# Performance work log

Hardware: AMD Instinct MI355X
Metric: run time of the kernel (lower is better)

Reference implementation:

```python
import jax, jax.numpy as jnp
import numpy as np
from jax import lax

N = 50000      # nodes
E = 1600000    # edges
F = 128        # input features
G = 32         # gnn_hidden_dim
H = 50         # lstm hidden_dim
SEQ = 10       # sequence_length


def setup_inputs() -> dict:
    key = jax.random.key(0)
    ks = jax.random.split(key, 12)
    s = 0.05
    return {
        "x": jax.random.normal(ks[0], (N, F), jnp.float32),
        "W_gcn": jax.random.normal(ks[1], (F, G), jnp.float32) * s,
        "b_gcn": jnp.zeros((G,), jnp.float32),
        "w_ih0": jax.random.normal(ks[2], (4 * H, G), jnp.float32) * s,
        "w_hh0": jax.random.normal(ks[3], (4 * H, H), jnp.float32) * s,
        "b_ih0": jnp.zeros((4 * H,), jnp.float32),
        "b_hh0": jnp.zeros((4 * H,), jnp.float32),
        "w_ih1": jax.random.normal(ks[4], (4 * H, H), jnp.float32) * s,
        "w_hh1": jax.random.normal(ks[5], (4 * H, H), jnp.float32) * s,
        "b_ih1": jnp.zeros((4 * H,), jnp.float32),
        "b_hh1": jnp.zeros((4 * H,), jnp.float32),
        "fc_w": jax.random.normal(ks[6], (1, H), jnp.float32) * s,
        "fc_b": jnp.zeros((1,), jnp.float32),
        "edge_index": jax.random.randint(ks[7], (2, E), 0, N, dtype=jnp.int64),
        "seq_len": SEQ,
    }


def gcn_conv(x, edge_index, W, b):
    # PyG GCNConv: add self-loops, symmetric deg^{-1/2} normalization,
    # linear transform, gather-scale-scatter aggregation at target nodes.
    n = x.shape[0]
    loop = jnp.arange(n, dtype=edge_index.dtype)
    src = jnp.concatenate([edge_index[0], loop])  # message sources j
    dst = jnp.concatenate([edge_index[1], loop])  # aggregation targets i
    deg = jax.ops.segment_sum(jnp.ones_like(dst, dtype=x.dtype), dst,
                              num_segments=n)
    dinv = jnp.where(deg > 0, lax.rsqrt(jnp.maximum(deg, 1.0)), 0.0)
    norm = dinv[src] * dinv[dst]                       # [E+N]
    h = x @ W                                          # [N, G]
    msg = h[src] * norm[:, None]                       # gather + scale
    out = jax.ops.segment_sum(msg, dst, num_segments=n)
    return out + b


def lstm_layer(x_proj, w_hh, b_hh):
    # x_proj: [T, B, 4H] precomputed input projections (i,f,g,o gate order).
    T, B, H4 = x_proj.shape
    Hd = H4 // 4
    h0 = jnp.zeros((B, Hd), x_proj.dtype)
    c0 = jnp.zeros((B, Hd), x_proj.dtype)

    def step(carry, xp):
        h, c = carry
        gates = xp + h @ w_hh.T + b_hh
        i, f, g, o = jnp.split(gates, 4, axis=-1)
        i, f, o = jax.nn.sigmoid(i), jax.nn.sigmoid(f), jax.nn.sigmoid(o)
        g = jnp.tanh(g)
        c = f * c + i * g
        h = o * jnp.tanh(c)
        return (h, c), h

    (h, c), ys = lax.scan(step, (h0, c0), x_proj)
    return ys, h


def reference(x, W_gcn, b_gcn, w_ih0, w_hh0, b_ih0, b_hh0,
              w_ih1, w_hh1, b_ih1, b_hh1, fc_w, fc_b,
              edge_index, seq_len):
    gnn_out = gcn_conv(x, edge_index, W_gcn, b_gcn)        # [N, G]
    # lstm_in = gnn_out repeated seq_len times -> input projection is
    # identical per step; compute once and broadcast (same math).
    p0 = gnn_out @ w_ih0.T + b_ih0                         # [N, 4H]
    x_proj0 = jnp.broadcast_to(p0, (seq_len,) + p0.shape)  # [T, N, 4H]
    ys0, _ = lstm_layer(x_proj0, w_hh0, b_hh0)             # [T, N, H]
    x_proj1 = ys0 @ w_ih1.T + b_ih1                        # [T, N, 4H]
    _, hn1 = lstm_layer(x_proj1, w_hh1, b_hh1)             # [N, H]
    return hn1 @ fc_w.T + fc_b                             # [N, 1]
```

## Files before the change

### kernel.cpp

```cpp
#include <hip/hip_runtime.h>
#include <hip/hip_bf16.h>

typedef __attribute__((ext_vector_type(8))) short short8;
typedef __attribute__((ext_vector_type(4))) float f32x4;

#define L2E 1.442695041f
#define SCAN_B 256

__device__ __forceinline__ short f2bf(float f) {
  union { __hip_bfloat16 b; short s; } u;
  u.b = __float2bfloat16(f);
  return u.s;
}
__device__ __forceinline__ float b2f(short s) {
  unsigned u = ((unsigned)(unsigned short)s) << 16;
  return __uint_as_float(u);
}

__device__ __forceinline__ float ldh(const float* p, size_t i) { return p[i]; }
__device__ __forceinline__ float ldh(const __hip_bfloat16* p, size_t i) {
  return __bfloat162float(p[i]);
}
__device__ __forceinline__ void sth(float* p, size_t i, float v) { p[i] = v; }
__device__ __forceinline__ void sth(__hip_bfloat16* p, size_t i, float v) {
  p[i] = __float2bfloat16(v);
}

__device__ __forceinline__ short8 load_gfrag(const float* g, size_t base) {
  const float4* gp = (const float4*)(g + base);
  float4 a = gp[0], b = gp[1];
  short8 t;
  t[0]=f2bf(a.x); t[1]=f2bf(a.y); t[2]=f2bf(a.z); t[3]=f2bf(a.w);
  t[4]=f2bf(b.x); t[5]=f2bf(b.y); t[6]=f2bf(b.z); t[7]=f2bf(b.w);
  return t;
}
__device__ __forceinline__ short8 load_gfrag(const __hip_bfloat16* g, size_t base) {
  return *(const short8*)(g + base);
}

#define OFF_WIH0 0
#define OFF_WHH0 13312
#define OFF_WIH1 39936
#define OFF_WHH1 66560
#define OFF_B0   93184
#define OFF_B1   94016
#define OFF_FCW  94848
#define IMG_BYTES 95104

__global__ void k_detect(const int* __restrict__ ei, int E, int* __restrict__ flag) {
  if (threadIdx.x == 0 && blockIdx.x == 0) {
    int odd_nz = 0, even_nz = 0;
    int m = min(128, E);
    for (int i = 0; i < m; ++i) {
      odd_nz |= (ei[2 * i + 1] != 0);
      even_nz |= (ei[2 * i] != 0);
    }
    *flag = (even_nz && !odd_nz) ? 1 : 0;
  }
}


__global__ void k_count(const int* __restrict__ ei, int E,
                        const int* __restrict__ flag, int* __restrict__ cnt) {
  int e = blockIdx.x * blockDim.x + threadIdx.x;
  if (e < E) {
    int d = (*flag) ? ei[2 * (E + e)] : ei[E + e];
    atomicAdd(&cnt[d], 1);
  }
}

__global__ void k_convert(const int* __restrict__ ei, int E,
                          unsigned int* __restrict__ ed, int* __restrict__ cnt) {
  __shared__ int sflag;
  if (threadIdx.x == 0) {
    int odd_nz = 0, even_nz = 0;
    int m = min(128, E);
    for (int i = 0; i < m; ++i) {
      odd_nz |= (ei[2 * i + 1] != 0);
      even_nz |= (ei[2 * i] != 0);
    }
    sflag = (even_nz && !odd_nz) ? 1 : 0;
  }
  __syncthreads();
  int is64 = sflag;
  int e = blockIdx.x * blockDim.x + threadIdx.x;
  if (e < E) {
    int s = is64 ? ei[2 * e] : ei[e];
    int d = is64 ? ei[2 * (E + e)] : ei[E + e];
    ed[e] = (unsigned int)s | ((unsigned int)d << 16);
    atomicAdd(&cnt[d], 1);
  }
}

__global__ void k_dinv(const int* __restrict__ cnt, float* __restrict__ dinv, int N) {
  int i = blockIdx.x * blockDim.x + threadIdx.x;
  if (i < N) dinv[i] = rsqrtf((float)cnt[i] + 1.0f);
}

__global__ __launch_bounds__(256) void k_scanA(const int* __restrict__ cnt,
                                               float* __restrict__ dinv,
                                               int* __restrict__ bsum, int N) {
  __shared__ int red[256];
  int b = blockIdx.x, t = threadIdx.x;
  int chunk = (N + SCAN_B - 1) / SCAN_B;
  int lo = b * chunk, hi = min(lo + chunk, N);
  int s = 0;
  for (int i = lo + t; i < hi; i += 256) {
    int c = cnt[i];
    dinv[i] = rsqrtf((float)c + 1.0f);
    s += c;
  }
  red[t] = s;
  __syncthreads();
  for (int o = 128; o > 0; o >>= 1) {
    if (t < o) red[t] += red[t + o];
    __syncthreads();
  }
  if (t == 0) bsum[b] = red[0];
}

__global__ __launch_bounds__(256) void k_scanB(int* __restrict__ a,
                                               const int* __restrict__ bsum,
                                               int N) {
  __shared__ int sh[256];
  int b = blockIdx.x, t = threadIdx.x;
  int chunk = (N + SCAN_B - 1) / SCAN_B;
  int lo = b * chunk, hi = min(lo + chunk, N);
  sh[t] = bsum[t];
  __syncthreads();
  for (int o = 1; o < 256; o <<= 1) {
    int u = (t >= o) ? sh[t - o] : 0;
    __syncthreads();
    sh[t] += u;
    __syncthreads();
  }
  int carry = (b == 0) ? 0 : sh[b - 1];
  __syncthreads();
  for (int i0 = lo; i0 < hi; i0 += 256) {
    int i = i0 + t;
    int c = (i < hi) ? a[i] : 0;
    sh[t] = c;
    __syncthreads();
    for (int o = 1; o < 256; o <<= 1) {
      int u = (t >= o) ? sh[t - o] : 0;
      __syncthreads();
      sh[t] += u;
      __syncthreads();
    }
    if (i < hi) a[i] = carry + sh[t] - c;
    carry += sh[255];
    __syncthreads();
  }
}

__global__ void k_fill_p(const unsigned int* __restrict__ ed, int E,
                         int* __restrict__ rowst,
                         unsigned short* __restrict__ csr, int lo, int hi) {
  int e = blockIdx.x * blockDim.x + threadIdx.x;
  if (e < E) {
    unsigned int v = ed[e];
    int d = (int)(v >> 16);
    if (d >= lo && d < hi) {
      int p = atomicAdd(&rowst[d], 1);
      csr[p] = (unsigned short)(v & 0xFFFFu);
    }
  }
}

template <typename CT>
__global__ void k_fill(const int* __restrict__ ei, int E,
                       const int* __restrict__ flag,
                       int* __restrict__ rowst, CT* __restrict__ csr,
                       int lo, int hi) {
  int e = blockIdx.x * blockDim.x + threadIdx.x;
  if (e < E) {
    int is64 = *flag;
    int d = is64 ? ei[2 * (E + e)] : ei[E + e];
    if (d >= lo && d < hi) {
      int s = is64 ? ei[2 * e] : ei[e];
      int p = atomicAdd(&rowst[d], 1);
      csr[p] = (CT)s;
    }
  }
}

template <typename HT>
__global__ __launch_bounds__(256) void k_hs(const float* __restrict__ x,
                                            const float* __restrict__ Wg,
                                            const float* __restrict__ dinv,
                                            HT* __restrict__ hs, int N) {
  __shared__ __align__(16) float xt[64][132];
  __shared__ __align__(16) float Wl[128][32];
  int tid = threadIdx.x;
  int nb = blockIdx.x * 64;
  for (int i = tid; i < 4096; i += 256) Wl[i >> 5][i & 31] = Wg[i];
  const float4* xv = (const float4*)x;
  for (int i = tid; i < 2048; i += 256) {
    int r = i >> 5, c = i & 31;
    float4 v = make_float4(0.f, 0.f, 0.f, 0.f);
    if (nb + r < N) v = xv[(size_t)(nb + r) * 32 + c];
    *(float4*)&xt[r][c * 4] = v;
  }
  __syncthreads();
  int nl = tid >> 2, gq = (tid & 3) * 8;
  float a[8];
#pragma unroll
  for (int j = 0; j < 8; ++j) a[j] = 0.f;
  for (int k = 0; k < 128; ++k) {
    float xk = xt[nl][k];
#pragma unroll
    for (int j = 0; j < 8; ++j) a[j] += xk * Wl[k][gq + j];
  }
  int n = nb + nl;
  if (n < N) {
    float d = dinv[n];
#pragma unroll
    for (int j = 0; j < 8; ++j) sth(hs, (size_t)n * 32 + gq + j, a[j] * d);
  }
}

template <typename HT, typename GT, typename CT>
__global__ void k_gather(const CT* __restrict__ csr, const int* __restrict__ rowst,
                         const HT* __restrict__ hs, const float* __restrict__ dinv,
                         const float* __restrict__ bg, GT* __restrict__ gout,
                         int N) {
  int w = (blockIdx.x * blockDim.x + threadIdx.x) >> 6;
  if (w >= N) return;
  int l = threadIdx.x & 63;
  int g = l & 31, j = l >> 5;
  int end = rowst[w];
  int start = (w == 0) ? 0 : rowst[w - 1];
  int deg = end - start;
  int dmax = min(deg, 64);
  int idx = (l < deg) ? (int)csr[start + l] : 0;
  float acc = 0.0f;
#pragma unroll 1
  for (int base = 0; base < 64; base += 16) {
    if (base >= dmax) break;
#pragma unroll
    for (int i = 0; i < 8; ++i) {
      int e = base + 2 * i + j;
      int src = __shfl(idx, e);
      float v = ldh(hs, (size_t)src * 32 + g);
      acc += (e < dmax) ? v : 0.0f;
    }
  }
  for (int k = start + 64 + j; k < end; k += 2)
    acc += ldh(hs, (size_t)csr[k] * 32 + g);
  acc += __shfl_xor(acc, 32);
  if (j == 0) {
    float v = (acc + ldh(hs, (size_t)w * 32 + g)) * dinv[w] + bg[g];
    sth(gout, (size_t)w * 32 + g, v);
  }
}

template <typename HT>
__global__ void k_scatter(const int* __restrict__ ei, int E,
                          const int* __restrict__ flag,
                          const HT* __restrict__ hs, float* __restrict__ gout) {
  long long gid = (long long)blockIdx.x * blockDim.x + threadIdx.x;
  int e = (int)(gid >> 3), part = (int)(gid & 7);
  if (e >= E) return;
  int is64 = *flag;
  int s = is64 ? ei[2 * e] : ei[e];
  int d = is64 ? ei[2 * (E + e)] : ei[E + e];
  int b = part * 4;
  float* gp = gout + (size_t)d * 32 + b;
  size_t hp = (size_t)s * 32 + b;
  atomicAdd(gp + 0, ldh(hs, hp + 0));
  atomicAdd(gp + 1, ldh(hs, hp + 1));
  atomicAdd(gp + 2, ldh(hs, hp + 2));
  atomicAdd(gp + 3, ldh(hs, hp + 3));
}
template <typename HT>
__global__ void k_finish(const HT* __restrict__ hs, const float* __restrict__ dinv,
                         const float* __restrict__ bg, float* __restrict__ gout,
                         int N) {
  int gid = blockIdx.x * blockDim.x + threadIdx.x;
  if (gid < N * 32) {
    int n = gid >> 5, g = gid & 31;
    gout[gid] = (gout[gid] + ldh(hs, (size_t)gid)) * dinv[n] + bg[g];
  }
}

__global__ void k_prep(const float* __restrict__ wih0, const float* __restrict__ whh0,
                       const float* __restrict__ wih1, const float* __restrict__ whh1,
                       const float* __restrict__ bih0, const float* __restrict__ bhh0,
                       const float* __restrict__ bih1, const float* __restrict__ bhh1,
                       const float* __restrict__ fcw, unsigned char* __restrict__ img,
                       int* __restrict__ rowst, int N) {
  int gid = blockIdx.x * blockDim.x + threadIdx.x;
  int nthr = gridDim.x * blockDim.x;
  for (int i = gid; i < N; i += nthr) rowst[i] = 0;
  {
    short* W = (short*)(img + OFF_WIH0);
    for (int i = gid; i < 208 * 32; i += nthr) {
      int row = i >> 5, k = i & 31, u = row >> 2, q = row & 3;
      float sc = (q == 2) ? 2.0f * L2E : -L2E;
      float v = (u < 50) ? wih0[(q * 50 + u) * 32 + k] * sc : 0.0f;
      W[row * 32 + (k ^ ((row & 3) << 3))] = f2bf(v);
    }
  }
  {
    short* W = (short*)(img + OFF_WHH0);
    for (int i = gid; i < 208 * 64; i += nthr) {
      int row = i >> 6, k = i & 63, u = row >> 2, q = row & 3;
      float sc = (q == 2) ? 2.0f * L2E : -L2E;
      float v = (u < 50 && k < 50) ? whh0[(q * 50 + u) * 50 + k] * sc : 0.0f;
      W[row * 64 + (k ^ ((row & 7) << 3))] = f2bf(v);
    }
  }
  {
    short* W = (short*)(img + OFF_WIH1);
    for (int i = gid; i < 208 * 64; i += nthr) {
      int row = i >> 6, k = i & 63, u = row >> 2, q = row & 3;
      float sc = (q == 2) ? 2.0f * L2E : -L2E;
      float v = (u < 50 && k < 50) ? wih1[(q * 50 + u) * 50 + k] * sc : 0.0f;
      W[row * 64 + (k ^ ((row & 7) << 3))] = f2bf(v);
    }
  }
  {
    short* W = (short*)(img + OFF_WHH1);
    for (int i = gid; i < 208 * 64; i += nthr) {
      int row = i >> 6, k = i & 63, u = row >> 2, q = row & 3;
      float sc = (q == 2) ? 2.0f * L2E : -L2E;
      float v = (u < 50 && k < 50) ? whh1[(q * 50 + u) * 50 + k] * sc : 0.0f;
      W[row * 64 + (k ^ ((row & 7) << 3))] = f2bf(v);
    }
  }
  {
    float* B = (float*)(img + OFF_B0);
    for (int i = gid; i < 208; i += nthr) {
      int u = i >> 2, q = i & 3;
      float sc = (q == 2) ? 2.0f * L2E : -L2E;
      B[i] = (u < 50) ? (bih0[q * 50 + u] + bhh0[q * 50 + u]) * sc : 0.0f;
    }
  }
  {
    float* B = (float*)(img + OFF_B1);
    for (int i = gid; i < 208; i += nthr) {
      int u = i >> 2, q = i & 3;
      float sc = (q == 2) ? 2.0f * L2E : -L2E;
      B[i] = (u < 50) ? (bih1[q * 50 + u] + bhh1[q * 50 + u]) * sc : 0.0f;
    }
  }
  {
    float* F = (float*)(img + OFF_FCW);
    for (int i = gid; i < 64; i += nthr) F[i] = (i < 50) ? fcw[i] : 0.0f;
  }
}

__device__ __forceinline__ float gate_update(const f32x4& acc, float& cp) {
  float ei = __builtin_amdgcn_exp2f(acc[0]);
  float ef = __builtin_amdgcn_exp2f(acc[1]);
  float eo = __builtin_amdgcn_exp2f(acc[3]);
  float eg = __builtin_amdgcn_exp2f(fminf(acc[2], 80.0f));
  float a = 1.0f + ei, b = 1.0f + ef;
  float rif = __builtin_amdgcn_rcpf(a * b);
  float iv = rif * b, fv = rif * a;
  float o1 = 1.0f + eo, g1 = eg + 1.0f;
  float rog = __builtin_amdgcn_rcpf(o1 * g1);
  float ov = rog * g1;
  float gv = (eg - 1.0f) * (rog * o1);
  float c = fv * cp + iv * gv;
  cp = c;
  float Ec = __builtin_amdgcn_exp2f(c * (2.0f * L2E));
  float th = (Ec - 1.0f) * __builtin_amdgcn_rcpf(Ec + 1.0f);
  return ov * th;
}

template <typename GT>
__global__ __launch_bounds__(512, 2) void k_lstm(const GT* __restrict__ gout,
    const unsigned char* __restrict__ img, const float* __restrict__ fcb_p,
    float* __restrict__ out, int N) {
  __shared__ __align__(16) unsigned char smem[160640];
  const int tid = threadIdx.x;
  {
    const uint4* s = (const uint4*)img;
    uint4* d = (uint4*)smem;
    for (int i = tid; i < IMG_BYTES / 16; i += 512) d[i] = s[i];
  }
  __syncthreads();
  const int lane = tid & 63, wid = tid >> 6;
  const int l15 = lane & 15, l4 = lane >> 4;
  const int swz7 = (l15 & 7) << 3, swz3 = (l15 & 3) << 3;
  const int node0 = blockIdx.x * 256 + wid * 32;

  const short* WIH0 = (const short*)(smem + OFF_WIH0);
  const short* WHH0 = (const short*)(smem + OFF_WHH0);
  const short* WIH1 = (const short*)(smem + OFF_WIH1);
  const short* WHH1 = (const short*)(smem + OFF_WHH1);
  const float* B0   = (const float*)(smem + OFF_B0);
  const float* B1   = (const float*)(smem + OFF_B1);
  const float* FCW  = (const float*)(smem + OFF_FCW);
  short* h0st = (short*)(smem + IMG_BYTES + wid * 8192);
  short* h1st = h0st + 2048;

  {
    uint4 z; z.x = z.y = z.z = z.w = 0u;
    uint4* p = (uint4*)h0st;
    for (int i = lane; i < 512; i += 64) p[i] = z;
  }

  f32x4 p0r[13][2];
  {
    short8 gfrag[2];
#pragma unroll
    for (int v = 0; v < 2; ++v) {
      int node = node0 + v * 16 + l15;
      short8 t = {0, 0, 0, 0, 0, 0, 0, 0};
      if (node < N) t = load_gfrag(gout, (size_t)node * 32 + l4 * 8);
      gfrag[v] = t;
    }
#pragma unroll
    for (int t = 0; t < 13; ++t) {
      short8 w = *(const short8*)(WIH0 + (16 * t + l15) * 32 + ((l4 * 8) ^ swz3));
      f32x4 bv = *(const f32x4*)(B0 + t * 16 + l4 * 4);
#pragma unroll
      for (int v = 0; v < 2; ++v)
        p0r[t][v] = __builtin_amdgcn_mfma_f32_16x16x32_bf16(w, gfrag[v], bv, 0, 0, 0);
    }
  }

  float c0[13][2], c1[13][2];
#pragma unroll
  for (int t = 0; t < 13; ++t) { c0[t][0]=0.f; c0[t][1]=0.f; c1[t][0]=0.f; c1[t][1]=0.f; }

#pragma unroll 1
  for (int s = 0; s < 10; ++s) {
    short8 h0f[2][2], h1f[2][2];
#pragma unroll
    for (int c = 0; c < 2; ++c)
#pragma unroll
      for (int v = 0; v < 2; ++v) {
        int nl = v * 16 + l15;
        h0f[c][v] = *(const short8*)(h0st + nl * 64 + ((c * 32 + l4 * 8) ^ swz7));
        h1f[c][v] = *(const short8*)(h1st + nl * 64 + ((c * 32 + l4 * 8) ^ swz7));
      }
#pragma unroll
    for (int t = 0; t < 13; ++t) {
      int arow = (16 * t + l15);
      short8 ah0 = *(const short8*)(WHH0 + arow * 64 + ((l4 * 8) ^ swz7));
      short8 ah1 = *(const short8*)(WHH0 + arow * 64 + ((32 + l4 * 8) ^ swz7));
#pragma unroll
      for (int v = 0; v < 2; ++v) {
        f32x4 acc = p0r[t][v];
        acc = __builtin_amdgcn_mfma_f32_16x16x32_bf16(ah0, h0f[0][v], acc, 0, 0, 0);
        acc = __builtin_amdgcn_mfma_f32_16x16x32_bf16(ah1, h0f[1][v], acc, 0, 0, 0);
        float h = gate_update(acc, c0[t][v]);
        h0st[(v * 16 + l15) * 64 + ((4 * t + l4) ^ swz7)] = f2bf(h);
      }
    }
    short8 h0nf[2][2];
#pragma unroll
    for (int c = 0; c < 2; ++c)
#pragma unroll
      for (int v = 0; v < 2; ++v) {
        int nl = v * 16 + l15;
        h0nf[c][v] = *(const short8*)(h0st + nl * 64 + ((c * 32 + l4 * 8) ^ swz7));
      }
#pragma unroll
    for (int t = 0; t < 13; ++t) {
      f32x4 bv = *(const f32x4*)(B1 + t * 16 + l4 * 4);
      int arow = (16 * t + l15);
      short8 ai0 = *(const short8*)(WIH1 + arow * 64 + ((l4 * 8) ^ swz7));
      short8 ai1 = *(const short8*)(WIH1 + arow * 64 + ((32 + l4 * 8) ^ swz7));
      short8 ah0 = *(const short8*)(WHH1 + arow * 64 + ((l4 * 8) ^ swz7));
      short8 ah1 = *(const short8*)(WHH1 + arow * 64 + ((32 + l4 * 8) ^ swz7));
#pragma unroll
      for (int v = 0; v < 2; ++v) {
        f32x4 acc = bv;
        acc = __builtin_amdgcn_mfma_f32_16x16x32_bf16(ai0, h0nf[0][v], acc, 0, 0, 0);
        acc = __builtin_amdgcn_mfma_f32_16x16x32_bf16(ai1, h0nf[1][v], acc, 0, 0, 0);
        acc = __builtin_amdgcn_mfma_f32_16x16x32_bf16(ah0, h1f[0][v], acc, 0, 0, 0);
        acc = __builtin_amdgcn_mfma_f32_16x16x32_bf16(ah1, h1f[1][v], acc, 0, 0, 0);
        float h = gate_update(acc, c1[t][v]);
        h1st[(v * 16 + l15) * 64 + ((4 * t + l4) ^ swz7)] = f2bf(h);
      }
    }
  }
  float fcb = fcb_p[0];
#pragma unroll
  for (int v = 0; v < 2; ++v) {
    int nl = v * 16 + l15;
    float facc = 0.f;
#pragma unroll
    for (int c = 0; c < 2; ++c) {
      short8 f = *(const short8*)(h1st + nl * 64 + ((c * 32 + l4 * 8) ^ swz7));
#pragma unroll
      for (int j = 0; j < 8; ++j)
        facc += b2f(f[j]) * FCW[c * 32 + l4 * 8 + j];
    }
    facc += __shfl_xor(facc, 16);
    facc += __shfl_xor(facc, 32);
    int node = node0 + v * 16 + l15;
    if (l4 == 0 && node < N) out[node] = facc + fcb;
  }
}

extern "C" void kernel_launch(void* const* d_in, const int* in_sizes, int n_in,
                              void* d_out, int out_size, void* d_ws, size_t ws_size,
                              hipStream_t stream) {
  const float* x    = (const float*)d_in[0];
  const float* Wg   = (const float*)d_in[1];
  const float* bg   = (const float*)d_in[2];
  const float* wih0 = (const float*)d_in[3];
  const float* whh0 = (const float*)d_in[4];
  const float* bih0 = (const float*)d_in[5];
  const float* bhh0 = (const float*)d_in[6];
  const float* wih1 = (const float*)d_in[7];
  const float* whh1 = (const float*)d_in[8];
  const float* bih1 = (const float*)d_in[9];
  const float* bhh1 = (const float*)d_in[10];
  const float* fcw  = (const float*)d_in[11];
  const float* fcb  = (const float*)d_in[12];
  const int*   edge = (const int*)d_in[13];
  int N = in_sizes[0] / 128;
  int E = in_sizes[13] / 2;

  char* ws = (char*)d_ws;
  size_t off = 0;
  auto take = [&](size_t b) {
    size_t o = off;
    off = (off + b + 255) & ~(size_t)255;
    return o;
  };
  int*   rowst = (int*)(ws + take((size_t)N * 4));
  float* dinv  = (float*)(ws + take((size_t)N * 4));
  int*   flag  = (int*)(ws + take(256));
  unsigned char* wimg = (unsigned char*)(ws + take(IMG_BYTES));
  size_t base = off;

  const int NP = 2;
  int span = (N + NP - 1) / NP;
  bool canU16 = (N <= 65535) && (E <= 100000000);

  size_t csr_b  = ((size_t)E * 2 + 255) & ~(size_t)255;
  size_t hsb    = ((size_t)N * 64 + 255) & ~(size_t)255;
  size_t reg2_b = (size_t)E * 4 > 2 * hsb ? (size_t)E * 4 : 2 * hsb;
  size_t needP  = base + csr_b + reg2_b;
  size_t needA = base + (((size_t)N * 128 + 255) & ~(size_t)255)
               + (((size_t)E * 4 + 255) & ~(size_t)255)
               + ((size_t)N * 128);

  k_prep<<<52, 256, 0, stream>>>(wih0, whh0, wih1, whh1, bih0, bhh0, bih1, bhh1,
                                 fcw, wimg, rowst, N);

  if (ws_size >= needA) {
    float* gout = (float*)(ws + take((size_t)N * 128));
    int*   csr  = (int*)(ws + take((size_t)E * 4));
    float* hs   = (float*)(ws + take((size_t)N * 128));
    int*   bsum = (int*)csr;
    k_detect<<<1, 1, 0, stream>>>(edge, E, flag);
    k_count<<<(E + 255) / 256, 256, 0, stream>>>(edge, E, flag, rowst);
    k_scanA<<<SCAN_B, 256, 0, stream>>>(rowst, dinv, bsum, N);
    k_scanB<<<SCAN_B, 256, 0, stream>>>(rowst, bsum, N);
    k_hs<float><<<(N + 63) / 64, 256, 0, stream>>>(x, Wg, dinv, hs, N);
    for (int p = 0; p < NP; ++p) {
      int lo = p * span, hi = min(lo + span, N);
      if (lo >= hi) break;
      k_fill<int><<<(E + 255) / 256, 256, 0, stream>>>(edge, E, flag, rowst,
                                                       csr, lo, hi);
    }
    k_gather<float, float, int><<<(N + 3) / 4, 256, 0, stream>>>(
        csr, rowst, hs, dinv, bg, gout, N);
    k_lstm<float><<<(N + 255) / 256, 512, 0, stream>>>(gout, wimg, fcb,
                                                       (float*)d_out, N);
  } else if (canU16 && ws_size >= needP) {
    unsigned short* csr = (unsigned short*)(ws + take(csr_b));
    char* reg2 = ws + take(reg2_b);
    unsigned int*   ed   = (unsigned int*)reg2;
    __hip_bfloat16* hs   = (__hip_bfloat16*)reg2;
    __hip_bfloat16* gout = (__hip_bfloat16*)(reg2 + hsb);
    int* bsum = (int*)csr;

    k_convert<<<(E + 255) / 256, 256, 0, stream>>>(edge, E, ed, rowst);
    k_scanA<<<SCAN_B, 256, 0, stream>>>(rowst, dinv, bsum, N);
    k_scanB<<<SCAN_B, 256, 0, stream>>>(rowst, bsum, N);
    for (int p = 0; p < NP; ++p) {
      int lo = p * span, hi = min(lo + span, N);
      if (lo >= hi) break;
      k_fill_p<<<(E + 255) / 256, 256, 0, stream>>>(ed, E, rowst, csr, lo, hi);
    }
    k_hs<__hip_bfloat16><<<(N + 63) / 64, 256, 0, stream>>>(x, Wg, dinv, hs, N);
    k_gather<__hip_bfloat16, __hip_bfloat16, unsigned short>
        <<<(N + 3) / 4, 256, 0, stream>>>(csr, rowst, hs, dinv, bg, gout, N);
    k_lstm<__hip_bfloat16><<<(N + 255) / 256, 512, 0, stream>>>(gout, wimg, fcb,
                                                                (float*)d_out, N);
  } else {
    float* gout = (float*)(ws + take((size_t)N * 128));
    __hip_bfloat16* hs = (__hip_bfloat16*)(ws + take((size_t)N * 64));
    hipMemsetAsync(gout, 0, (size_t)N * 128, stream);
    k_detect<<<1, 1, 0, stream>>>(edge, E, flag);
    k_count<<<(E + 255) / 256, 256, 0, stream>>>(edge, E, flag, rowst);
    k_dinv<<<(N + 255) / 256, 256, 0, stream>>>(rowst, dinv, N);
    k_hs<__hip_bfloat16><<<(N + 63) / 64, 256, 0, stream>>>(x, Wg, dinv, hs, N);
    int sc_blocks = (int)(((long long)E * 8 + 255) / 256);
    k_scatter<__hip_bfloat16><<<sc_blocks, 256, 0, stream>>>(edge, E, flag, hs, gout);
    k_finish<__hip_bfloat16><<<(N * 32 + 255) / 256, 256, 0, stream>>>(
        hs, dinv, bg, gout, N);
    k_lstm<float><<<(N + 255) / 256, 512, 0, stream>>>(gout, wimg, fcb,
                                                       (float*)d_out, N);
  }
}
```

Measured before the change: 349.9 us.

## Fuse CSR build into cooperative kernel, process four nodes per gather wave

Replaces the convert, two scan kernels and the partitioned fill launches with a single cooperative kernel that uses grid-wide syncs between the count, degree/dinv, prefix-scan and fill phases. This removes several launches and the gaps between them. The gather kernel now handles four destination nodes per wave, sharing one rowst load and shuffling the row bounds. The fill partition count rises from 2 to 4, and the compact u16/bf16 path is now preferred over the fp32 path whenever N fits. Risks include grid.sync cost on 512 blocks, a serial prefix over bsum in every block, and lower bf16 precision on the chosen path.

```diff
diff --git a/kernel.cpp b/kernel.cpp
--- a/kernel.cpp
+++ b/kernel.cpp
@@ -1,5 +1,8 @@
 #include <hip/hip_runtime.h>
 #include <hip/hip_bf16.h>
+#include <hip/hip_cooperative_groups.h>
+
+namespace cg = cooperative_groups;
 
 typedef __attribute__((ext_vector_type(8))) short short8;
 typedef __attribute__((ext_vector_type(4))) float f32x4;
@@ -56,6 +59,105 @@
       even_nz |= (ei[2 * i] != 0);
     }
     *flag = (even_nz && !odd_nz) ? 1 : 0;
+  }
+}
+
+__global__ __launch_bounds__(256) void k_edges(const int* __restrict__ ei,
+    int E, int N, int* __restrict__ rowst, float* __restrict__ dinv,
+    int* __restrict__ bsum, unsigned int* __restrict__ ed,
+    unsigned short* __restrict__ csr, int NP) {
+  cg::grid_group grid = cg::this_grid();
+  const int tid = threadIdx.x, b = blockIdx.x, GB = gridDim.x;
+  const int T = GB * 256;
+  const int gid = b * 256 + tid;
+  __shared__ int sh[256];
+  __shared__ int sflag;
+
+  for (int i = gid; i < N; i += T) rowst[i] = 0;
+  if (tid == 0) {
+    int odd_nz = 0, even_nz = 0;
+    int m = min(128, E);
+    for (int i = 0; i < m; ++i) {
+      odd_nz |= (ei[2 * i + 1] != 0);
+      even_nz |= (ei[2 * i] != 0);
+    }
+    sflag = (even_nz && !odd_nz) ? 1 : 0;
+  }
+  __syncthreads();
+  int is64 = sflag;
+  grid.sync();
+
+  for (int e = gid; e < E; e += T) {
+    int s = is64 ? ei[2 * e] : ei[e];
+    int d = is64 ? ei[2 * (E + e)] : ei[E + e];
+    ed[e] = (unsigned int)s | ((unsigned int)d << 16);
+    atomicAdd(&rowst[d], 1);
+  }
+  grid.sync();
+
+  const int chunk = (N + GB - 1) / GB;
+  const int lo = b * chunk, hi = min(lo + chunk, N);
+  {
+    int s = 0;
+    for (int i = lo + tid; i < hi; i += 256) {
+      int c = rowst[i];
+      dinv[i] = rsqrtf((float)c + 1.0f);
+      s += c;
+    }
+    sh[tid] = s;
+    __syncthreads();
+    for (int o = 128; o > 0; o >>= 1) {
+      if (tid < o) sh[tid] += sh[tid + o];
+      __syncthreads();
+    }
+    if (tid == 0) bsum[b] = sh[0];
+    __syncthreads();
+  }
+  grid.sync();
+
+  {
+    int part = 0;
+    for (int i = tid; i < b; i += 256) part += bsum[i];
+    sh[tid] = part;
+    __syncthreads();
+    for (int o = 128; o > 0; o >>= 1) {
+      if (tid < o) sh[tid] += sh[tid + o];
+      __syncthreads();
+    }
+    int carry = sh[0];
+    __syncthreads();
+    for (int i0 = lo; i0 < hi; i0 += 256) {
+      int i = i0 + tid;
+      int c = (i < hi) ? rowst[i] : 0;
+      sh[tid] = c;
+      __syncthreads();
+      for (int o = 1; o < 256; o <<= 1) {
+        int u = (tid >= o) ? sh[tid - o] : 0;
+        __syncthreads();
+        sh[tid] += u;
+        __syncthreads();
+      }
+      if (i < hi) rowst[i] = carry + sh[tid] - c;
+      carry += sh[255];
+      __syncthreads();
+    }
+  }
+  grid.sync();
+
+  const int span = (N + NP - 1) / NP;
+  for (int p = 0; p < NP; ++p) {
+    int wlo = p * span, whi = min(wlo + span, N);
+    if (wlo < whi) {
+      for (int e = gid; e < E; e += T) {
+        unsigned int v = ed[e];
+        int d = (int)(v >> 16);
+        if (d >= wlo && d < whi) {
+          int pos = atomicAdd(&rowst[d], 1);
+          csr[pos] = (unsigned short)(v & 0xFFFFu);
+        }
+      }
+    }
+    if (p + 1 < NP) grid.sync();
   }
 }
 
@@ -220,37 +322,54 @@
 }
 
 template <typename HT, typename GT, typename CT>
-__global__ void k_gather(const CT* __restrict__ csr, const int* __restrict__ rowst,
-                         const HT* __restrict__ hs, const float* __restrict__ dinv,
-                         const float* __restrict__ bg, GT* __restrict__ gout,
-                         int N) {
-  int w = (blockIdx.x * blockDim.x + threadIdx.x) >> 6;
-  if (w >= N) return;
+__global__ void k_gather4(const CT* __restrict__ csr, const int* __restrict__ rowst,
+                          const HT* __restrict__ hs, const float* __restrict__ dinv,
+                          const float* __restrict__ bg, GT* __restrict__ gout,
+                          int N) {
+  long long gtid = (long long)blockIdx.x * blockDim.x + threadIdx.x;
+  int wave = (int)(gtid >> 6);
+  int n0 = wave * 4;
+  if (n0 >= N) return;
   int l = threadIdx.x & 63;
-  int g = l & 31, j = l >> 5;
-  int end = rowst[w];
-  int start = (w == 0) ? 0 : rowst[w - 1];
-  int deg = end - start;
-  int dmax = min(deg, 64);
-  int idx = (l < deg) ? (int)csr[start + l] : 0;
-  float acc = 0.0f;
+  int gf = l & 31, j = l >> 5;
+  int rr = 0;
+  int ri = n0 - 1 + l;
+  if (l <= 4 && ri >= 0 && ri < N) rr = rowst[ri];
+  int st[4], en[4], idx[4], deg[4];
+#pragma unroll
+  for (int q = 0; q < 4; ++q) {
+    st[q] = __shfl(rr, q);
+    en[q] = __shfl(rr, q + 1);
+    deg[q] = en[q] - st[q];
+  }
+#pragma unroll
+  for (int q = 0; q < 4; ++q)
+    idx[q] = (n0 + q < N && l < deg[q]) ? (int)csr[st[q] + l] : 0;
+  float bgv = bg[gf];
+#pragma unroll
+  for (int q = 0; q < 4; ++q) {
+    int w = n0 + q;
+    if (w >= N) break;
+    float acc = 0.f;
+    int dm = min(deg[q], 64);
 #pragma unroll 1
-  for (int base = 0; base < 64; base += 16) {
-    if (base >= dmax) break;
-#pragma unroll
-    for (int i = 0; i < 8; ++i) {
-      int e = base + 2 * i + j;
-      int src = __shfl(idx, e);
-      float v = ldh(hs, (size_t)src * 32 + g);
-      acc += (e < dmax) ? v : 0.0f;
-    }
-  }
-  for (int k = start + 64 + j; k < end; k += 2)
-    acc += ldh(hs, (size_t)csr[k] * 32 + g);
-  acc += __shfl_xor(acc, 32);
-  if (j == 0) {
-    float v = (acc + ldh(hs, (size_t)w * 32 + g)) * dinv[w] + bg[g];
-    sth(gout, (size_t)w * 32 + g, v);
+    for (int base = 0; base < 64; base += 16) {
+      if (base >= dm) break;
+#pragma unroll
+      for (int i = 0; i < 8; ++i) {
+        int e = base + 2 * i + j;
+        int src = __shfl(idx[q], e);
+        float v = ldh(hs, (size_t)src * 32 + gf);
+        acc += (e < dm) ? v : 0.f;
+      }
+    }
+    for (int k2 = st[q] + 64 + j; k2 < en[q]; k2 += 2)
+      acc += ldh(hs, (size_t)csr[k2] * 32 + gf);
+    acc += __shfl_xor(acc, 32);
+    if (j == 0) {
+      float v = (acc + ldh(hs, (size_t)w * 32 + gf)) * dinv[w] + bgv;
+      sth(gout, (size_t)w * 32 + gf, v);
+    }
   }
 }
 
@@ -531,7 +650,7 @@
   unsigned char* wimg = (unsigned char*)(ws + take(IMG_BYTES));
   size_t base = off;
 
-  const int NP = 2;
+  const int NP = 4;
   int span = (N + NP - 1) / NP;
   bool canU16 = (N <= 65535) && (E <= 100000000);
 
@@ -543,10 +662,19 @@
                + (((size_t)E * 4 + 255) & ~(size_t)255)
                + ((size_t)N * 128);
 
+  int coop = 0;
+  {
+    int dev = 0;
+    hipDeviceProp_t prop;
+    if (hipGetDevice(&dev) == hipSuccess &&
+        hipGetDeviceProperties(&prop, dev) == hipSuccess)
+      coop = prop.cooperativeLaunch;
+  }
+
   k_prep<<<52, 256, 0, stream>>>(wih0, whh0, wih1, whh1, bih0, bhh0, bih1, bhh1,
                                  fcw, wimg, rowst, N);
 
-  if (ws_size >= needA) {
+  if (ws_size >= needA && !canU16) {
     float* gout = (float*)(ws + take((size_t)N * 128));
     int*   csr  = (int*)(ws + take((size_t)E * 4));
     float* hs   = (float*)(ws + take((size_t)N * 128));
@@ -562,7 +690,8 @@
       k_fill<int><<<(E + 255) / 256, 256, 0, stream>>>(edge, E, flag, rowst,
                                                        csr, lo, hi);
     }
-    k_gather<float, float, int><<<(N + 3) / 4, 256, 0, stream>>>(
+    int gwaves = (N + 3) / 4;
+    k_gather4<float, float, int><<<(gwaves * 64 + 255) / 256, 256, 0, stream>>>(
         csr, rowst, hs, dinv, bg, gout, N);
     k_lstm<float><<<(N + 255) / 256, 512, 0, stream>>>(gout, wimg, fcb,
                                                        (float*)d_out, N);
@@ -574,19 +703,51 @@
     __hip_bfloat16* gout = (__hip_bfloat16*)(reg2 + hsb);
     int* bsum = (int*)csr;
 
-    k_convert<<<(E + 255) / 256, 256, 0, stream>>>(edge, E, ed, rowst);
+    if (coop) {
+      int NPc = NP;
+      void* kargs[] = { (void*)&edge, (void*)&E, (void*)&N, (void*)&rowst,
+                        (void*)&dinv, (void*)&bsum, (void*)&ed, (void*)&csr,
+                        (void*)&NPc };
+      hipLaunchCooperativeKernel((void*)k_edges, dim3(512), dim3(256), kargs,
+                                 0, stream);
+    } else {
+      k_convert<<<(E + 255) / 256, 256, 0, stream>>>(edge, E, ed, rowst);
+      k_scanA<<<SCAN_B, 256, 0, stream>>>(rowst, dinv, bsum, N);
+      k_scanB<<<SCAN_B, 256, 0, stream>>>(rowst, bsum, N);
+      for (int p = 0; p < NP; ++p) {
+        int lo = p * span, hi = min(lo + span, N);
+        if (lo >= hi) break;
+        k_fill_p<<<(E + 255) / 256, 256, 0, stream>>>(ed, E, rowst, csr, lo, hi);
+      }
+    }
+    k_hs<__hip_bfloat16><<<(N + 63) / 64, 256, 0, stream>>>(x, Wg, dinv, hs, N);
+    int gwaves = (N + 3) / 4;
+    k_gather4<__hip_bfloat16, __hip_bfloat16, unsigned short>
+        <<<(gwaves * 64 + 255) / 256, 256, 0, stream>>>(csr, rowst, hs, dinv,
+                                                        bg, gout, N);
+    k_lstm<__hip_bfloat16><<<(N + 255) / 256, 512, 0, stream>>>(gout, wimg, fcb,
+                                                                (float*)d_out, N);
+  } else if (ws_size >= needA) {
+    float* gout = (float*)(ws + take((size_t)N * 128));
+    int*   csr  = (int*)(ws + take((size_t)E * 4));
+    float* hs   = (float*)(ws + take((size_t)N * 128));
+    int*   bsum = (int*)csr;
+    k_detect<<<1, 1, 0, stream>>>(edge, E, flag);
+    k_count<<<(E + 255) / 256, 256, 0, stream>>>(edge, E, flag, rowst);
     k_scanA<<<SCAN_B, 256, 0, stream>>>(rowst, dinv, bsum, N);
     k_scanB<<<SCAN_B, 256, 0, stream>>>(rowst, bsum, N);
+    k_hs<float><<<(N + 63) / 64, 256, 0, stream>>>(x, Wg, dinv, hs, N);
     for (int p = 0; p < NP; ++p) {
       int lo = p * span, hi = min(lo + span, N);
       if (lo >= hi) break;
-      k_fill_p<<<(E + 255) / 256, 256, 0, stream>>>(ed, E, rowst, csr, lo, hi);
-    }
-    k_hs<__hip_bfloat16><<<(N + 63) / 64, 256, 0, stream>>>(x, Wg, dinv, hs, N);
-    k_gather<__hip_bfloat16, __hip_bfloat16, unsigned short>
-        <<<(N + 3) / 4, 256, 0, stream>>>(csr, rowst, hs, dinv, bg, gout, N);
-    k_lstm<__hip_bfloat16><<<(N + 255) / 256, 512, 0, stream>>>(gout, wimg, fcb,
-                                                                (float*)d_out, N);
+      k_fill<int><<<(E + 255) / 256, 256, 0, stream>>>(edge, E, flag, rowst,
+                                                       csr, lo, hi);
+    }
+    int gwaves = (N + 3) / 4;
+    k_gather4<float, float, int><<<(gwaves * 64 + 255) / 256, 256, 0, stream>>>(
+        csr, rowst, hs, dinv, bg, gout, N);
+    k_lstm<float><<<(N + 255) / 256, 512, 0, stream>>>(gout, wimg, fcb,
+                                                       (float*)d_out, N);
   } else {
     float* gout = (float*)(ws + take((size_t)N * 128));
     __hip_bfloat16* hs = (__hip_bfloat16*)(ws + take((size_t)N * 64));
```

After: 710.5 us. +103.0%, slower.

## Prefer compact bf16/u16 CSR path, process four nodes per gather wave

Applied to the files above, without the earlier changes.

Reorders path selection so the compact path (u16 CSR indices, bf16 node features) runs whenever N fits in 16 bits and workspace allows, rather than the fp32/int32 path. The gather kernel now handles four destination nodes per wavefront, loading row offsets once via shuffles and prefetching each node's neighbour indices. The CSR fill is split into four passes instead of two. This aims to cut memory traffic and per-node launch granularity, at the cost of bf16 rounding of intermediate features and more fill passes over the edge list.

```diff
diff --git a/kernel.cpp b/kernel.cpp
--- a/kernel.cpp
+++ b/kernel.cpp
@@ -220,37 +220,54 @@
 }
 
 template <typename HT, typename GT, typename CT>
-__global__ void k_gather(const CT* __restrict__ csr, const int* __restrict__ rowst,
-                         const HT* __restrict__ hs, const float* __restrict__ dinv,
-                         const float* __restrict__ bg, GT* __restrict__ gout,
-                         int N) {
-  int w = (blockIdx.x * blockDim.x + threadIdx.x) >> 6;
-  if (w >= N) return;
+__global__ void k_gather4(const CT* __restrict__ csr, const int* __restrict__ rowst,
+                          const HT* __restrict__ hs, const float* __restrict__ dinv,
+                          const float* __restrict__ bg, GT* __restrict__ gout,
+                          int N) {
+  long long gtid = (long long)blockIdx.x * blockDim.x + threadIdx.x;
+  int wave = (int)(gtid >> 6);
+  int n0 = wave * 4;
+  if (n0 >= N) return;
   int l = threadIdx.x & 63;
-  int g = l & 31, j = l >> 5;
-  int end = rowst[w];
-  int start = (w == 0) ? 0 : rowst[w - 1];
-  int deg = end - start;
-  int dmax = min(deg, 64);
-  int idx = (l < deg) ? (int)csr[start + l] : 0;
-  float acc = 0.0f;
+  int gf = l & 31, j = l >> 5;
+  int rr = 0;
+  int ri = n0 - 1 + l;
+  if (l <= 4 && ri >= 0 && ri < N) rr = rowst[ri];
+  int st[4], en[4], idx[4], deg[4];
+#pragma unroll
+  for (int q = 0; q < 4; ++q) {
+    st[q] = __shfl(rr, q);
+    en[q] = __shfl(rr, q + 1);
+    deg[q] = en[q] - st[q];
+  }
+#pragma unroll
+  for (int q = 0; q < 4; ++q)
+    idx[q] = (n0 + q < N && l < deg[q]) ? (int)csr[st[q] + l] : 0;
+  float bgv = bg[gf];
+#pragma unroll
+  for (int q = 0; q < 4; ++q) {
+    int w = n0 + q;
+    if (w >= N) break;
+    float acc = 0.f;
+    int dm = min(deg[q], 64);
 #pragma unroll 1
-  for (int base = 0; base < 64; base += 16) {
-    if (base >= dmax) break;
-#pragma unroll
-    for (int i = 0; i < 8; ++i) {
-      int e = base + 2 * i + j;
-      int src = __shfl(idx, e);
-      float v = ldh(hs, (size_t)src * 32 + g);
-      acc += (e < dmax) ? v : 0.0f;
-    }
-  }
-  for (int k = start + 64 + j; k < end; k += 2)
-    acc += ldh(hs, (size_t)csr[k] * 32 + g);
-  acc += __shfl_xor(acc, 32);
-  if (j == 0) {
-    float v = (acc + ldh(hs, (size_t)w * 32 + g)) * dinv[w] + bg[g];
-    sth(gout, (size_t)w * 32 + g, v);
+    for (int base = 0; base < 64; base += 16) {
+      if (base >= dm) break;
+#pragma unroll
+      for (int i = 0; i < 8; ++i) {
+        int e = base + 2 * i + j;
+        int src = __shfl(idx[q], e);
+        float v = ldh(hs, (size_t)src * 32 + gf);
+        acc += (e < dm) ? v : 0.f;
+      }
+    }
+    for (int k2 = st[q] + 64 + j; k2 < en[q]; k2 += 2)
+      acc += ldh(hs, (size_t)csr[k2] * 32 + gf);
+    acc += __shfl_xor(acc, 32);
+    if (j == 0) {
+      float v = (acc + ldh(hs, (size_t)w * 32 + gf)) * dinv[w] + bgv;
+      sth(gout, (size_t)w * 32 + gf, v);
+    }
   }
 }
 
@@ -531,7 +548,7 @@
   unsigned char* wimg = (unsigned char*)(ws + take(IMG_BYTES));
   size_t base = off;
 
-  const int NP = 2;
+  const int NP = 4;
   int span = (N + NP - 1) / NP;
   bool canU16 = (N <= 65535) && (E <= 100000000);
 
@@ -546,7 +563,30 @@
   k_prep<<<52, 256, 0, stream>>>(wih0, whh0, wih1, whh1, bih0, bhh0, bih1, bhh1,
                                  fcw, wimg, rowst, N);
 
-  if (ws_size >= needA) {
+  if (canU16 && ws_size >= needP) {
+    unsigned short* csr = (unsigned short*)(ws + take(csr_b));
+    char* reg2 = ws + take(reg2_b);
+    unsigned int*   ed   = (unsigned int*)reg2;
+    __hip_bfloat16* hs   = (__hip_bfloat16*)reg2;
+    __hip_bfloat16* gout = (__hip_bfloat16*)(reg2 + hsb);
+    int* bsum = (int*)csr;
+
+    k_convert<<<(E + 255) / 256, 256, 0, stream>>>(edge, E, ed, rowst);
+    k_scanA<<<SCAN_B, 256, 0, stream>>>(rowst, dinv, bsum, N);
+    k_scanB<<<SCAN_B, 256, 0, stream>>>(rowst, bsum, N);
+    for (int p = 0; p < NP; ++p) {
+      int lo = p * span, hi = min(lo + span, N);
+      if (lo >= hi) break;
+      k_fill_p<<<(E + 255) / 256, 256, 0, stream>>>(ed, E, rowst, csr, lo, hi);
+    }
+    k_hs<__hip_bfloat16><<<(N + 63) / 64, 256, 0, stream>>>(x, Wg, dinv, hs, N);
+    int gwaves = (N + 3) / 4;
+    k_gather4<__hip_bfloat16, __hip_bfloat16, unsigned short>
+        <<<(gwaves * 64 + 255) / 256, 256, 0, stream>>>(csr, rowst, hs, dinv,
+                                                        bg, gout, N);
+    k_lstm<__hip_bfloat16><<<(N + 255) / 256, 512, 0, stream>>>(gout, wimg, fcb,
+                                                                (float*)d_out, N);
+  } else if (ws_size >= needA) {
     float* gout = (float*)(ws + take((size_t)N * 128));
     int*   csr  = (int*)(ws + take((size_t)E * 4));
     float* hs   = (float*)(ws + take((size_t)N * 128));
@@ -562,31 +602,11 @@
       k_fill<int><<<(E + 255) / 256, 256, 0, stream>>>(edge, E, flag, rowst,
                                                        csr, lo, hi);
     }
-    k_gather<float, float, int><<<(N + 3) / 4, 256, 0, stream>>>(
+    int gwaves = (N + 3) / 4;
+    k_gather4<float, float, int><<<(gwaves * 64 + 255) / 256, 256, 0, stream>>>(
         csr, rowst, hs, dinv, bg, gout, N);
     k_lstm<float><<<(N + 255) / 256, 512, 0, stream>>>(gout, wimg, fcb,
                                                        (float*)d_out, N);
-  } else if (canU16 && ws_size >= needP) {
-    unsigned short* csr = (unsigned short*)(ws + take(csr_b));
-    char* reg2 = ws + take(reg2_b);
-    unsigned int*   ed   = (unsigned int*)reg2;
-    __hip_bfloat16* hs   = (__hip_bfloat16*)reg2;
-    __hip_bfloat16* gout = (__hip_bfloat16*)(reg2 + hsb);
-    int* bsum = (int*)csr;
-
-    k_convert<<<(E + 255) / 256, 256, 0, stream>>>(edge, E, ed, rowst);
-    k_scanA<<<SCAN_B, 256, 0, stream>>>(rowst, dinv, bsum, N);
-    k_scanB<<<SCAN_B, 256, 0, stream>>>(rowst, bsum, N);
-    for (int p = 0; p < NP; ++p) {
-      int lo = p * span, hi = min(lo + span, N);
-      if (lo >= hi) break;
-      k_fill_p<<<(E + 255) / 256, 256, 0, stream>>>(ed, E, rowst, csr, lo, hi);
-    }
-    k_hs<__hip_bfloat16><<<(N + 63) / 64, 256, 0, stream>>>(x, Wg, dinv, hs, N);
-    k_gather<__hip_bfloat16, __hip_bfloat16, unsigned short>
-        <<<(N + 3) / 4, 256, 0, stream>>>(csr, rowst, hs, dinv, bg, gout, N);
-    k_lstm<__hip_bfloat16><<<(N + 255) / 256, 512, 0, stream>>>(gout, wimg, fcb,
-                                                                (float*)d_out, N);
   } else {
     float* gout = (float*)(ws + take((size_t)N * 128));
     __hip_bfloat16* hs = (__hip_bfloat16*)(ws + take((size_t)N * 64));
```

After: 323.1 us, median of 2. 1.08x faster.
